# Performance work log

Hardware: AMD Instinct MI355X
Metric: run time of the kernel (lower is better)

The kernel has to match this reference:

```python
import jax, jax.numpy as jnp
import numpy as np

B, C_IN, C_OUT, H, W = 16, 128, 256, 80, 80
K, STRIDE, PAD = 3, 2, 1
KK = K * K
HO = (H + 2 * PAD - K) // STRIDE + 1
WO = (W + 2 * PAD - K) // STRIDE + 1


def setup_inputs() -> dict:
    key = jax.random.key(0)
    ks = jax.random.split(key, 3)
    x = jax.random.normal(ks[0], (B, C_IN, H, W), jnp.float32)
    offset_w = jax.random.normal(ks[1], (2 * KK, C_IN), jnp.float32) * 0.01
    offset_b = jnp.zeros((2 * KK,), jnp.float32)
    deform_w = jax.random.normal(ks[2], (C_OUT, C_IN, K, K), jnp.float32) * (1.0 / np.sqrt(C_IN * KK))
    deform_b = jnp.zeros((C_OUT,), jnp.float32)
    bn_gamma = jnp.ones((C_OUT,), jnp.float32)
    bn_beta = jnp.zeros((C_OUT,), jnp.float32)
    return dict(x=x, offset_w=offset_w, offset_b=offset_b, deform_w=deform_w,
                deform_b=deform_b, bn_gamma=bn_gamma, bn_beta=bn_beta)


def _bilinear_gather(x, py, px):
    # x: [B,C,H,W]; py,px: [B,KK,HO,WO] float sample coords; zero-pad outside.
    Bb, C, Hh, Ww = x.shape
    y0 = jnp.floor(py)
    x0 = jnp.floor(px)
    wy1 = py - y0
    wx1 = px - x0
    y0i = y0.astype(jnp.int32)
    x0i = x0.astype(jnp.int32)
    flat = x.reshape(Bb, C, Hh * Ww)

    def gather(yi, xi):
        valid = (yi >= 0) & (yi < Hh) & (xi >= 0) & (xi < Ww)
        idx = jnp.clip(yi, 0, Hh - 1) * Ww + jnp.clip(xi, 0, Ww - 1)
        g = jax.vmap(lambda f, i: f[:, i])(flat, idx.reshape(Bb, -1))
        g = g.reshape(Bb, C, *yi.shape[1:])
        return g * valid[:, None].astype(x.dtype)

    g00 = gather(y0i, x0i)
    g01 = gather(y0i, x0i + 1)
    g10 = gather(y0i + 1, x0i)
    g11 = gather(y0i + 1, x0i + 1)
    wy1 = wy1[:, None]  # [B,1,KK,HO,WO]
    wx1 = wx1[:, None]
    wy0 = 1.0 - wy1
    wx0 = 1.0 - wx1
    return wy0 * (wx0 * g00 + wx1 * g01) + wy1 * (wx0 * g10 + wx1 * g11)


def reference(x, offset_w, offset_b, deform_w, deform_b, bn_gamma, bn_beta):
    Bb = x.shape[0]
    # offset conv: 1x1, stride 2 (H,W even -> simple subsample)
    xs = x[:, :, ::2, ::2]  # [B,C,HO,WO]
    off = jnp.einsum('oc,bchw->bohw', offset_w, xs) + offset_b[None, :, None, None]
    off = off.reshape(Bb, KK, 2, HO, WO)  # torchvision layout: (dy,dx) per kernel tap
    dy, dx = off[:, :, 0], off[:, :, 1]
    ky = (jnp.arange(KK) // K).astype(jnp.float32)
    kx = (jnp.arange(KK) % K).astype(jnp.float32)
    base_y = (jnp.arange(HO) * STRIDE - PAD).astype(jnp.float32)
    base_x = (jnp.arange(WO) * STRIDE - PAD).astype(jnp.float32)
    py = base_y[None, None, :, None] + ky[None, :, None, None] + dy
    px = base_x[None, None, None, :] + kx[None, :, None, None] + dx
    sampled = _bilinear_gather(x, py, px)  # [B,C,KK,HO,WO]
    w = deform_w.reshape(C_OUT, C_IN * KK)
    out = jnp.einsum('ok,bkhw->bohw', w, sampled.reshape(Bb, C_IN * KK, HO, WO))
    out = out + deform_b[None, :, None, None]
    # BatchNorm2d in training mode (batch stats, biased var, eps=1e-5)
    mean = out.mean(axis=(0, 2, 3))
    var = out.var(axis=(0, 2, 3))
    out = (out - mean[None, :, None, None]) * jax.lax.rsqrt(var + 1e-5)[None, :, None, None]
    out = out * bn_gamma[None, :, None, None] + bn_beta[None, :, None, None]
    # SiLU
    return out * jax.nn.sigmoid(out)
```

## Files before the change

### kernel.cpp

```cpp
#include <hip/hip_runtime.h>
#include <hip/hip_bf16.h>

#define B_    16
#define CIN_  128
#define COUT_ 256
#define H_    80
#define W_    80
#define HO_   40
#define WO_   40
#define KK_   9
#define SK_   1152
#define NPIX_ 25600
#define NKS_  36

typedef __attribute__((ext_vector_type(8))) short short8;
typedef __attribute__((ext_vector_type(4))) float floatx4;

__device__ __forceinline__ unsigned short f2bu(float v) {
  __hip_bfloat16 h = __float2bfloat16(v);
  return *reinterpret_cast<unsigned short*>(&h);
}
__device__ __forceinline__ float bu2f(unsigned short u) {
  return __uint_as_float(((unsigned)u) << 16);
}
__device__ __forceinline__ unsigned int pk2(float a, float b) {
  return (unsigned)f2bu(a) | ((unsigned)f2bu(b) << 16);
}
__device__ __forceinline__ void gl_lds16(const unsigned short* g, unsigned short* l) {
  __builtin_amdgcn_global_load_lds(
      (const __attribute__((address_space(1))) unsigned int*)(const void*)g,
      (__attribute__((address_space(3))) unsigned int*)(void*)l, 16, 0, 0);
}

__global__ __launch_bounds__(256) void k_pack(const float* __restrict__ dw,
                                              unsigned short* __restrict__ Apk) {
  int t = blockIdx.x * 256 + threadIdx.x;
  int j  = t & 7;
  int qd = (t >> 3) & 3;
  int m  = (t >> 5) & 255;
  int ks = t >> 13;
  int k  = ks * 32 + qd * 8 + j;
  int kk = k >> 7, ci = k & 127;
  Apk[t] = f2bu(dw[m * SK_ + ci * KK_ + kk]);
}

__global__ __launch_bounds__(256) void k_cl(const float* __restrict__ x,
                                            const float* __restrict__ ow,
                                            const float* __restrict__ ob,
                                            unsigned short* __restrict__ xcl,
                                            float* __restrict__ off) {
  __shared__ unsigned int ts[CIN_ * 41];
  __shared__ float owl[18 * CIN_];
  __shared__ float obl[18];
  const int tid = threadIdx.x;
  const int bid = blockIdx.x;
  const int xcd = bid & 7;
  const int i0_ = bid >> 3;
  const int b   = (i0_ / 80) * 8 + xcd;
  const int y   = i0_ % 80;
  const bool even = (y & 1) == 0;

  for (int j = tid; j < CIN_ * 20; j += 256) {
    int ci = j / 20, xq = j % 20;
    float4 v = *(const float4*)&x[(((size_t)b * CIN_ + ci) * H_ + y) * W_ + xq * 4];
    ts[ci * 41 + xq * 2 + 0] = pk2(v.x, v.y);
    ts[ci * 41 + xq * 2 + 1] = pk2(v.z, v.w);
  }
  if (even) {
    for (int j = tid; j < 18 * CIN_; j += 256) owl[j] = ow[j];
    if (tid < 18) obl[tid] = ob[tid];
  }
  __syncthreads();

  unsigned short* op = xcl + ((size_t)b * H_ * W_ + (size_t)y * W_) * CIN_;
  for (int j = tid; j < 40 * 32; j += 256) {
    int xw = j >> 5, cg = j & 31;
    unsigned w0 = ts[(cg * 4 + 0) * 41 + xw];
    unsigned w1 = ts[(cg * 4 + 1) * 41 + xw];
    unsigned w2 = ts[(cg * 4 + 2) * 41 + xw];
    unsigned w3 = ts[(cg * 4 + 3) * 41 + xw];
    uint2 lo = make_uint2((w0 & 0xFFFFu) | (w1 << 16),
                          (w2 & 0xFFFFu) | (w3 << 16));
    uint2 hi = make_uint2((w0 >> 16) | (w1 & 0xFFFF0000u),
                          (w2 >> 16) | (w3 & 0xFFFF0000u));
    *(uint2*)(op + (size_t)(2 * xw) * CIN_ + cg * 4)     = lo;
    *(uint2*)(op + (size_t)(2 * xw + 1) * CIN_ + cg * 4) = hi;
  }

  if (even) {
    const int ho = y >> 1;
    for (int i = tid; i < 18 * WO_; i += 256) {
      int o = i / WO_, wo = i - o * WO_;
      float acc = obl[o];
      const float* wr = &owl[o * CIN_];
#pragma unroll 4
      for (int ci = 0; ci < CIN_; ci++)
        acc += wr[ci] * bu2f((unsigned short)(ts[ci * 41 + wo] & 0xFFFFu));
      off[((b * 18 + o) * HO_ + ho) * WO_ + wo] = acc;
    }
  }
}

__global__ __launch_bounds__(256) void k_sample_cl(const unsigned short* __restrict__ xcl,
                                                   const float* __restrict__ off,
                                                   unsigned short* __restrict__ Spk) {
  __shared__ __align__(16) int   pidx[80 * 4];
  __shared__ __align__(16) float pw[80 * 4];
  const int tid = threadIdx.x;
  const int j0   = blockIdx.x;
  const int xcd  = j0 & 7;
  const int s    = j0 >> 3;
  const int b_hi = s / 180;
  const int t0   = s % 180;
  const int g    = t0 / 9;
  const int kk   = t0 % 9;
  const int b    = b_hi * 8 + xcd;
  const int ho0  = g * 2;

  if (tid < 80) {
    int hop = tid / 40, px = tid % 40;
    int ho = ho0 + hop;
    float dy = off[((b * 18 + 2 * kk) * HO_ + ho) * WO_ + px];
    float dx = off[((b * 18 + 2 * kk + 1) * HO_ + ho) * WO_ + px];
    float py  = (float)(2 * ho - 1 + (kk / 3)) + dy;
    float pxf = (float)(2 * px - 1 + (kk % 3)) + dx;
    float y0f = floorf(py), x0f = floorf(pxf);
    float wy1 = py - y0f, wx1 = pxf - x0f;
    float wy0 = 1.f - wy1, wx0 = 1.f - wx1;
    int y0 = (int)y0f, x0 = (int)x0f;
    int y1 = y0 + 1, x1 = x0 + 1;
    bool vy0 = (y0 >= 0) && (y0 < H_);
    bool vy1 = (y1 >= 0) && (y1 < H_);
    bool vx0 = (x0 >= 0) && (x0 < W_);
    bool vx1 = (x1 >= 0) && (x1 < W_);
    int y0c = min(max(y0, 0), H_ - 1), y1c = min(max(y1, 0), H_ - 1);
    int x0c = min(max(x0, 0), W_ - 1), x1c = min(max(x1, 0), W_ - 1);
    pidx[tid * 4 + 0] = (y0c * W_ + x0c) << 7;  pw[tid * 4 + 0] = (vy0 && vx0) ? wy0 * wx0 : 0.f;
    pidx[tid * 4 + 1] = (y0c * W_ + x1c) << 7;  pw[tid * 4 + 1] = (vy0 && vx1) ? wy0 * wx1 : 0.f;
    pidx[tid * 4 + 2] = (y1c * W_ + x0c) << 7;  pw[tid * 4 + 2] = (vy1 && vx0) ? wy1 * wx0 : 0.f;
    pidx[tid * 4 + 3] = (y1c * W_ + x1c) << 7;  pw[tid * 4 + 3] = (vy1 && vx1) ? wy1 * wx1 : 0.f;
  }
  __syncthreads();

  const unsigned short* xb = xcl + (size_t)b * (H_ * W_ * CIN_);
#pragma unroll
  for (int it = 0; it < 5; it++) {
    int i = it * 256 + tid;
    int oct = i & 15;
    int pxh = i >> 4;
    int4   I  = *(const int4*)&pidx[pxh * 4];
    float4 Wv = *(const float4*)&pw[pxh * 4];
    short8 c00 = *(const short8*)(xb + I.x + oct * 8);
    short8 c01 = *(const short8*)(xb + I.y + oct * 8);
    short8 c10 = *(const short8*)(xb + I.z + oct * 8);
    short8 c11 = *(const short8*)(xb + I.w + oct * 8);
    short8 r;
#pragma unroll
    for (int i2 = 0; i2 < 8; i2++) {
      float v = Wv.x * bu2f((unsigned short)c00[i2]) +
                Wv.y * bu2f((unsigned short)c01[i2]) +
                Wv.z * bu2f((unsigned short)c10[i2]) +
                Wv.w * bu2f((unsigned short)c11[i2]);
      r[i2] = (short)f2bu(v);
    }
    int p  = b * 1600 + (ho0 + (pxh / 40)) * 40 + (pxh % 40);
    int pt = p >> 4, lm = p & 15;
    int ks = kk * 4 + (oct >> 2);
    int qd = oct & 3;
    *(short8*)&Spk[(((size_t)pt * NKS_ + ks) * 64 + qd * 16 + lm) * 8] = r;
  }
}

__global__ __launch_bounds__(256) void k_gemm(const unsigned short* __restrict__ Apk,
                                              const unsigned short* __restrict__ Spk,
                                              float* __restrict__ c0,
                                              float* __restrict__ c1) {
  __shared__ __align__(16) unsigned short a_sh[2][2048];
  __shared__ __align__(16) unsigned short b_sh[2][2048];

  const int tid = threadIdx.x;
  const int wv = tid >> 6;
  const int ln = tid & 63;
  const int lm = ln & 15;
  const int qd = ln >> 4;

  const int bid = blockIdx.x;
  const int xcd = bid & 7;
  const int i   = bid >> 3;
  const int b   = xcd + 8 * (i / 200);
  const int r_  = i % 200;
  const int pxg = r_ >> 3;
  const int cq  = (r_ >> 1) & 3;
  const int ksp = r_ & 1;
  const int pt0 = b * 100 + pxg * 4;
  const int cbase = cq * 64;
  const int ks0 = ksp * 18;

  const unsigned short* agbase = Apk + (size_t)ks0 * 8192 + cbase * 32 + tid * 8;
  const unsigned short* bgbase = Spk + ((size_t)(pt0 + wv) * NKS_ + ks0) * 512 + ln * 8;

  floatx4 acc[4];
#pragma unroll
  for (int mt = 0; mt < 4; mt++) acc[mt] = (floatx4){0.f, 0.f, 0.f, 0.f};

  gl_lds16(agbase, &a_sh[0][0] + wv * 512);
  gl_lds16(bgbase, &b_sh[0][0] + wv * 512);
  __syncthreads();

  for (int ks = 0; ks < 18; ks++) {
    const int buf = ks & 1, nb = buf ^ 1;
    if (ks + 1 < 18) {
      gl_lds16(agbase + (size_t)(ks + 1) * 8192, &a_sh[nb][0] + wv * 512);
      gl_lds16(bgbase + (size_t)(ks + 1) * 512,  &b_sh[nb][0] + wv * 512);
    }
    const unsigned short* al = &a_sh[buf][0] + lm * 32 + qd * 8;
    const unsigned short* bl = &b_sh[buf][0] + wv * 512 + ln * 8;
    short8 a0 = *(const short8*)(al + 0 * 512);
    short8 a1 = *(const short8*)(al + 1 * 512);
    short8 a2 = *(const short8*)(al + 2 * 512);
    short8 a3 = *(const short8*)(al + 3 * 512);
    short8 bv = *(const short8*)(bl);
    acc[0] = __builtin_amdgcn_mfma_f32_16x16x32_bf16(a0, bv, acc[0], 0, 0, 0);
    acc[1] = __builtin_amdgcn_mfma_f32_16x16x32_bf16(a1, bv, acc[1], 0, 0, 0);
    acc[2] = __builtin_amdgcn_mfma_f32_16x16x32_bf16(a2, bv, acc[2], 0, 0, 0);
    acc[3] = __builtin_amdgcn_mfma_f32_16x16x32_bf16(a3, bv, acc[3], 0, 0, 0);
    __syncthreads();
  }

  const int p = (pt0 + wv) * 16 + lm;
  const int bb = p / 1600, rem = p % 1600;
  float* ob = (ksp ? c1 : c0) + (size_t)bb * COUT_ * 1600 + rem;
#pragma unroll
  for (int mt = 0; mt < 4; mt++) {
#pragma unroll
    for (int r = 0; r < 4; r++) {
      const int c = cbase + mt * 16 + qd * 4 + r;
      ob[(size_t)c * 1600] = acc[mt][r];
    }
  }
}

__global__ __launch_bounds__(256) void k_stats(const float* __restrict__ io0,
                                               const float* __restrict__ io1,
                                               float* __restrict__ accum) {
  const int c = blockIdx.x >> 2;
  const int q = blockIdx.x & 3;
  const int tid = threadIdx.x;
  float s1 = 0.f, s2 = 0.f;
  for (int i = q * (NPIX_ / 4) + tid; i < (q + 1) * (NPIX_ / 4); i += 256) {
    int b = i / 1600, r = i - b * 1600;
    size_t idx = ((size_t)b * COUT_ + c) * 1600 + r;
    float v = io0[idx] + io1[idx];
    s1 += v;
    s2 += v * v;
  }
#pragma unroll
  for (int d = 1; d < 64; d <<= 1) {
    s1 += __shfl_xor(s1, d, 64);
    s2 += __shfl_xor(s2, d, 64);
  }
  __shared__ float rs[4], rq[4];
  if ((tid & 63) == 0) { rs[tid >> 6] = s1; rq[tid >> 6] = s2; }
  __syncthreads();
  if (tid == 0) {
    atomicAdd(&accum[c],         rs[0] + rs[1] + rs[2] + rs[3]);
    atomicAdd(&accum[COUT_ + c], rq[0] + rq[1] + rq[2] + rq[3]);
  }
}

__global__ __launch_bounds__(256) void k_bn(float* __restrict__ io0,
                                            const float* __restrict__ io1,
                                            const float* __restrict__ accum,
                                            const float* __restrict__ gamma,
                                            const float* __restrict__ beta) {
  const int t = blockIdx.x * 256 + threadIdx.x;
  const int i0 = t * 4;
  const int c = (i0 / (HO_ * WO_)) % COUT_;
  const float mean = accum[c] * (1.f / NPIX_);
  const float var  = accum[COUT_ + c] * (1.f / NPIX_) - mean * mean;
  const float inv  = rsqrtf(var + 1e-5f);
  const float g  = gamma[c] * inv;
  const float be = beta[c] - mean * g;
  float4 r0 = *(const float4*)(io0 + i0);
  float4 r1 = *(const float4*)(io1 + i0);
  float v[4] = {r0.x + r1.x, r0.y + r1.y, r0.z + r1.z, r0.w + r1.w};
#pragma unroll
  for (int q = 0; q < 4; q++) {
    float u = v[q] * g + be;
    v[q] = u / (1.f + expf(-u));
  }
  *(float4*)(io0 + i0) = make_float4(v[0], v[1], v[2], v[3]);
}

extern "C" void kernel_launch(void* const* d_in, const int* in_sizes, int n_in,
                              void* d_out, int out_size, void* d_ws, size_t ws_size,
                              hipStream_t stream) {
  const float* x     = (const float*)d_in[0];
  const float* ow    = (const float*)d_in[1];
  const float* ob    = (const float*)d_in[2];
  const float* dw    = (const float*)d_in[3];
  const float* gamma = (const float*)d_in[5];
  const float* beta  = (const float*)d_in[6];
  float* out = (float*)d_out;

  float* off   = (float*)d_ws;
  float* accum = off + B_ * 18 * HO_ * WO_;
  unsigned short* Apk = (unsigned short*)(accum + 2 * COUT_);
  unsigned short* Spk = Apk + (size_t)SK_ * COUT_;
  unsigned short* xcl = Spk + (size_t)NPIX_ * SK_;
  float* c1 = (float*)xcl;

  hipMemsetAsync(accum, 0, 2 * COUT_ * sizeof(float), stream);
  k_pack<<<SK_, 256, 0, stream>>>(dw, Apk);
  k_cl<<<B_ * H_, 256, 0, stream>>>(x, ow, ob, xcl, off);
  k_sample_cl<<<B_ * KK_ * 20, 256, 0, stream>>>(xcl, off, Spk);
  k_gemm<<<3200, 256, 0, stream>>>(Apk, Spk, out, c1);
  k_stats<<<COUT_ * 4, 256, 0, stream>>>(out, c1, accum);
  k_bn<<<(NPIX_ * COUT_ / 4 + 255) / 256, 256, 0, stream>>>(
      out, c1, accum, gamma, beta);
}
```

Measured before the change: 195.5 us.

## Drop split-K in GEMM and fuse BN statistics into GEMM epilogue

The GEMM no longer splits K into two halves with separate partial outputs. Each block now runs the full 36-step K loop and writes a single output. The per-channel sum and sum-of-squares are reduced in the GEMM epilogue with shuffles and shared memory, then added to global accumulators atomically, which removes the separate stats kernel and the extra read of the partial buffer. The accumulator memset is folded into k_pack. The trade-off is half as many GEMM blocks, each with a longer serial K loop, plus more atomics.

```diff
diff --git a/kernel.cpp b/kernel.cpp
--- a/kernel.cpp
+++ b/kernel.cpp
@@ -33,7 +33,12 @@
 }
 
 __global__ __launch_bounds__(256) void k_pack(const float* __restrict__ dw,
-                                              unsigned short* __restrict__ Apk) {
+                                              unsigned short* __restrict__ Apk,
+                                              float* __restrict__ accum) {
+  if (blockIdx.x == 0) {
+    accum[threadIdx.x] = 0.f;
+    accum[256 + threadIdx.x] = 0.f;
+  }
   int t = blockIdx.x * 256 + threadIdx.x;
   int j  = t & 7;
   int qd = (t >> 3) & 3;
@@ -173,10 +178,11 @@
 
 __global__ __launch_bounds__(256) void k_gemm(const unsigned short* __restrict__ Apk,
                                               const unsigned short* __restrict__ Spk,
-                                              float* __restrict__ c0,
-                                              float* __restrict__ c1) {
+                                              float* __restrict__ outp,
+                                              float* __restrict__ accum) {
   __shared__ __align__(16) unsigned short a_sh[2][2048];
   __shared__ __align__(16) unsigned short b_sh[2][2048];
+  __shared__ float sF1[4][64], sF2[4][64];
 
   const int tid = threadIdx.x;
   const int wv = tid >> 6;
@@ -187,17 +193,15 @@
   const int bid = blockIdx.x;
   const int xcd = bid & 7;
   const int i   = bid >> 3;
-  const int b   = xcd + 8 * (i / 200);
-  const int r_  = i % 200;
-  const int pxg = r_ >> 3;
-  const int cq  = (r_ >> 1) & 3;
-  const int ksp = r_ & 1;
+  const int b   = xcd + 8 * (i / 100);
+  const int r_  = i % 100;
+  const int pxg = r_ >> 2;
+  const int cq  = r_ & 3;
   const int pt0 = b * 100 + pxg * 4;
   const int cbase = cq * 64;
-  const int ks0 = ksp * 18;
-
-  const unsigned short* agbase = Apk + (size_t)ks0 * 8192 + cbase * 32 + tid * 8;
-  const unsigned short* bgbase = Spk + ((size_t)(pt0 + wv) * NKS_ + ks0) * 512 + ln * 8;
+
+  const unsigned short* agbase = Apk + cbase * 32 + tid * 8;
+  const unsigned short* bgbase = Spk + (size_t)(pt0 + wv) * NKS_ * 512 + ln * 8;
 
   floatx4 acc[4];
 #pragma unroll
@@ -207,9 +211,9 @@
   gl_lds16(bgbase, &b_sh[0][0] + wv * 512);
   __syncthreads();
 
-  for (int ks = 0; ks < 18; ks++) {
+  for (int ks = 0; ks < NKS_; ks++) {
     const int buf = ks & 1, nb = buf ^ 1;
-    if (ks + 1 < 18) {
+    if (ks + 1 < NKS_) {
       gl_lds16(agbase + (size_t)(ks + 1) * 8192, &a_sh[nb][0] + wv * 512);
       gl_lds16(bgbase + (size_t)(ks + 1) * 512,  &b_sh[nb][0] + wv * 512);
     }
@@ -228,48 +232,45 @@
   }
 
   const int p = (pt0 + wv) * 16 + lm;
-  const int bb = p / 1600, rem = p % 1600;
-  float* ob = (ksp ? c1 : c0) + (size_t)bb * COUT_ * 1600 + rem;
+  float* ob = outp + (size_t)b * COUT_ * 1600 + (p - b * 1600);
+  float s1[16], s2[16];
 #pragma unroll
   for (int mt = 0; mt < 4; mt++) {
 #pragma unroll
     for (int r = 0; r < 4; r++) {
       const int c = cbase + mt * 16 + qd * 4 + r;
-      ob[(size_t)c * 1600] = acc[mt][r];
-    }
-  }
-}
-
-__global__ __launch_bounds__(256) void k_stats(const float* __restrict__ io0,
-                                               const float* __restrict__ io1,
-                                               float* __restrict__ accum) {
-  const int c = blockIdx.x >> 2;
-  const int q = blockIdx.x & 3;
-  const int tid = threadIdx.x;
-  float s1 = 0.f, s2 = 0.f;
-  for (int i = q * (NPIX_ / 4) + tid; i < (q + 1) * (NPIX_ / 4); i += 256) {
-    int b = i / 1600, r = i - b * 1600;
-    size_t idx = ((size_t)b * COUT_ + c) * 1600 + r;
-    float v = io0[idx] + io1[idx];
-    s1 += v;
-    s2 += v * v;
-  }
-#pragma unroll
-  for (int d = 1; d < 64; d <<= 1) {
-    s1 += __shfl_xor(s1, d, 64);
-    s2 += __shfl_xor(s2, d, 64);
-  }
-  __shared__ float rs[4], rq[4];
-  if ((tid & 63) == 0) { rs[tid >> 6] = s1; rq[tid >> 6] = s2; }
+      float v = acc[mt][r];
+      ob[(size_t)c * 1600] = v;
+      s1[mt * 4 + r] = v;
+      s2[mt * 4 + r] = v * v;
+    }
+  }
+#pragma unroll
+  for (int d = 1; d < 16; d <<= 1) {
+#pragma unroll
+    for (int i2 = 0; i2 < 16; i2++) {
+      s1[i2] += __shfl_xor(s1[i2], d, 64);
+      s2[i2] += __shfl_xor(s2[i2], d, 64);
+    }
+  }
+  if (lm == 0) {
+#pragma unroll
+    for (int i2 = 0; i2 < 16; i2++) {
+      int cl = (i2 >> 2) * 16 + qd * 4 + (i2 & 3);
+      sF1[wv][cl] = s1[i2];
+      sF2[wv][cl] = s2[i2];
+    }
+  }
   __syncthreads();
-  if (tid == 0) {
-    atomicAdd(&accum[c],         rs[0] + rs[1] + rs[2] + rs[3]);
-    atomicAdd(&accum[COUT_ + c], rq[0] + rq[1] + rq[2] + rq[3]);
-  }
-}
-
-__global__ __launch_bounds__(256) void k_bn(float* __restrict__ io0,
-                                            const float* __restrict__ io1,
+  if (tid < 64) {
+    float a1 = sF1[0][tid] + sF1[1][tid] + sF1[2][tid] + sF1[3][tid];
+    float a2 = sF2[0][tid] + sF2[1][tid] + sF2[2][tid] + sF2[3][tid];
+    atomicAdd(&accum[cbase + tid], a1);
+    atomicAdd(&accum[COUT_ + cbase + tid], a2);
+  }
+}
+
+__global__ __launch_bounds__(256) void k_bn(float* __restrict__ io,
                                             const float* __restrict__ accum,
                                             const float* __restrict__ gamma,
                                             const float* __restrict__ beta) {
@@ -281,15 +282,14 @@
   const float inv  = rsqrtf(var + 1e-5f);
   const float g  = gamma[c] * inv;
   const float be = beta[c] - mean * g;
-  float4 r0 = *(const float4*)(io0 + i0);
-  float4 r1 = *(const float4*)(io1 + i0);
-  float v[4] = {r0.x + r1.x, r0.y + r1.y, r0.z + r1.z, r0.w + r1.w};
+  float4 r = *(const float4*)(io + i0);
+  float v[4] = {r.x, r.y, r.z, r.w};
 #pragma unroll
   for (int q = 0; q < 4; q++) {
     float u = v[q] * g + be;
     v[q] = u / (1.f + expf(-u));
   }
-  *(float4*)(io0 + i0) = make_float4(v[0], v[1], v[2], v[3]);
+  *(float4*)(io + i0) = make_float4(v[0], v[1], v[2], v[3]);
 }
 
 extern "C" void kernel_launch(void* const* d_in, const int* in_sizes, int n_in,
@@ -308,14 +308,11 @@
   unsigned short* Apk = (unsigned short*)(accum + 2 * COUT_);
   unsigned short* Spk = Apk + (size_t)SK_ * COUT_;
   unsigned short* xcl = Spk + (size_t)NPIX_ * SK_;
-  float* c1 = (float*)xcl;
-
-  hipMemsetAsync(accum, 0, 2 * COUT_ * sizeof(float), stream);
-  k_pack<<<SK_, 256, 0, stream>>>(dw, Apk);
+
+  k_pack<<<SK_, 256, 0, stream>>>(dw, Apk, accum);
   k_cl<<<B_ * H_, 256, 0, stream>>>(x, ow, ob, xcl, off);
   k_sample_cl<<<B_ * KK_ * 20, 256, 0, stream>>>(xcl, off, Spk);
-  k_gemm<<<3200, 256, 0, stream>>>(Apk, Spk, out, c1);
-  k_stats<<<COUT_ * 4, 256, 0, stream>>>(out, c1, accum);
+  k_gemm<<<1600, 256, 0, stream>>>(Apk, Spk, out, accum);
   k_bn<<<(NPIX_ * COUT_ / 4 + 255) / 256, 256, 0, stream>>>(
-      out, c1, accum, gamma, beta);
-}
+      out, accum, gamma, beta);
+}
```

After: 200.6 us. 1.03x slower.
